# Performance work log

Hardware: AMD Instinct MI355X
Metric: run time of the kernel (lower is better)

## Reference

```python
import jax, jax.numpy as jnp
import numpy as np

B, R, E, H = 1024, 1024, 1024, 512
L_ATTR, L_OBJ, L_RELA = 16, 36, 64
EPS = 1e-8


def _lstm_cell(x, h, c, Wih, Whh, bih, bhh):
    # torch.nn.LSTMCell: gates ordered i, f, g, o
    g = x @ Wih.T + bih + h @ Whh.T + bhh
    i, f, gg, o = jnp.split(g, 4, axis=1)
    c2 = jax.nn.sigmoid(f) * c + jax.nn.sigmoid(i) * jnp.tanh(gg)
    h2 = jax.nn.sigmoid(o) * jnp.tanh(c2)
    return h2, c2


def _attend(h, feats, p_feats, mask, Wq, bq, wa, ba):
    att_h = h @ Wq.T + bq                         # [B,H]
    dot = jnp.tanh(p_feats + att_h[:, None, :])   # [B,L,H]
    scores = dot @ wa + ba                        # [B,L]
    w = jax.nn.softmax(scores, axis=1)
    w = w * mask
    w = w / (w.sum(1, keepdims=True) + EPS)
    return jnp.einsum('bl,bld->bd', w, feats)     # [B,R]


def setup_inputs() -> dict:
    key = jax.random.key(0)
    ks = iter(jax.random.split(key, 64))
    n = lambda shp, s=0.02: jax.random.normal(next(ks), shp, dtype=jnp.float32) * s
    inp = {
        'xt': n((B, E), 1.0), 'fc_feats': n((B, R), 1.0),
        'state_h': n((2, B, R), 1.0), 'state_c': n((2, B, R), 1.0),
        'attr_feats': n((B, L_ATTR, R), 1.0), 'obj_feats': n((B, L_OBJ, R), 1.0),
        'rela_feats': n((B, L_RELA, R), 1.0),
        'p_attr_feats': n((B, L_ATTR, H), 1.0), 'p_obj_feats': n((B, L_OBJ, H), 1.0),
        'p_rela_feats': n((B, L_RELA, H), 1.0),
        'attr_masks': jnp.ones((B, L_ATTR), jnp.float32),
        'att_masks': jnp.ones((B, L_OBJ), jnp.float32),
        'rela_masks': jnp.ones((B, L_RELA), jnp.float32),
        'att_Wih': n((4 * R, E + 2 * R)), 'att_Whh': n((4 * R, R)),
        'att_bih': n((4 * R,)), 'att_bhh': n((4 * R,)),
        'lang_Wih': n((4 * R, 4 * R)), 'lang_Whh': n((4 * R, R)),
        'lang_bih': n((4 * R,)), 'lang_bhh': n((4 * R,)),
    }
    for p in ('attr', 'obj', 'rela'):
        inp[p + '_Wq'] = n((H, R)); inp[p + '_bq'] = n((H,))
        inp[p + '_wa'] = n((H,));   inp[p + '_ba'] = n((1,))
    return inp


def reference(xt, fc_feats, state_h, state_c, attr_feats, obj_feats, rela_feats,
              p_attr_feats, p_obj_feats, p_rela_feats, attr_masks, att_masks,
              rela_masks, att_Wih, att_Whh, att_bih, att_bhh, lang_Wih, lang_Whh,
              lang_bih, lang_bhh, attr_Wq, attr_bq, attr_wa, attr_ba, obj_Wq,
              obj_bq, obj_wa, obj_ba, rela_Wq, rela_bq, rela_wa, rela_ba):
    prev_h = state_h[-1]
    att_in = jnp.concatenate([prev_h, fc_feats, xt], axis=1)
    h_att, c_att = _lstm_cell(att_in, state_h[0], state_c[0],
                              att_Wih, att_Whh, att_bih, att_bhh)
    a_attr = _attend(h_att, attr_feats, p_attr_feats, attr_masks,
                     attr_Wq, attr_bq, attr_wa, attr_ba)
    a_obj = _attend(h_att, obj_feats, p_obj_feats, att_masks,
                    obj_Wq, obj_bq, obj_wa, obj_ba)
    a_rela = _attend(h_att, rela_feats, p_rela_feats, rela_masks,
                     rela_Wq, rela_bq, rela_wa, rela_ba)
    lang_in = jnp.concatenate([h_att, a_attr, a_obj, a_rela], axis=1)
    h_lang, c_lang = _lstm_cell(lang_in, state_h[1], state_c[1],
                                lang_Wih, lang_Whh, lang_bih, lang_bhh)
    # dropout in eval mode -> identity
    output = h_lang
    return output, jnp.stack([h_att, h_lang]), jnp.stack([c_att, c_lang])
```

## Files before the change

kernel.cpp:

```cpp
#include <hip/hip_runtime.h>
#include <math.h>

typedef _Float16 half8  __attribute__((ext_vector_type(8)));
typedef _Float16 half4v __attribute__((ext_vector_type(4)));
typedef float    f32x4  __attribute__((ext_vector_type(4)));

__device__ __forceinline__ _Float16 f2h(float f) { return (_Float16)f; }

__device__ __forceinline__ float tanh_fast(float x) {
    float e = __expf(2.f * x);
    return 1.f - 2.f / (e + 1.f);
}

#define LDSB (128 * 40)

__device__ __forceinline__ void gemm_body(
    _Float16* __restrict__ sm,
    const float* A0, const float* A1, const float* A2p, const float* A3,
    const float* A4,
    const float* W0, const float* W1, const float* W2,
    int w0cols, int w0s, int w1s, int nsel,
    _Float16* __restrict__ Cpart, int ldc,
    int kb, int kLen, int ntile, int mtile, int zout)
{
    _Float16* smA = sm;
    _Float16* smW = sm + 2 * LDSB;
    const int tid  = threadIdx.x;
    const int lane = tid & 63;
    const int wid  = tid >> 6;
    const int wm   = wid >> 1, wn = wid & 1;
    const int m0   = mtile * 128;
    const int n0   = ntile * 128;
    const int nt   = kLen >> 5;
    const int srow = tid >> 3;
    const int scol = (tid & 7) << 2;
    const int fr   = lane & 15;
    const int kq   = lane >> 4;

    const float* wsel = nullptr;
    if (nsel) {
        int sel = n0 >> 9;
        const float* Wq = (sel == 0) ? W0 : (sel == 1) ? W1 : W2;
        wsel = Wq + (size_t)((n0 & 511) + srow) * 1024 + kb + scol;
    }

    f32x4 acc[4][4] = {};
    float4 va[4], vw[4];

    auto LOADA = [&](int lk) {
        int gk = kb + lk;
        int seg = gk >> 10;
        const float* ap = (seg == 0) ? A0 : (seg == 1) ? A1 : (seg == 2) ? A2p
                        : (seg == 3) ? A3 : A4;
        ap += (size_t)(m0 + srow) * 1024 + (gk & 1023) + scol;
        #pragma unroll
        for (int p = 0; p < 4; ++p)
            va[p] = *reinterpret_cast<const float4*>(ap + (size_t)p * 32 * 1024);
    };
    auto LOADW = [&](int lk) {
        const float* wp; int wstr;
        if (nsel) {
            wp = wsel + lk; wstr = 1024;
        } else {
            int gk = kb + lk;
            if (gk < w0cols) { wp = W0 + (size_t)(n0 + srow) * w0s + gk + scol;            wstr = w0s; }
            else             { wp = W1 + (size_t)(n0 + srow) * w1s + (gk - w0cols) + scol; wstr = w1s; }
        }
        #pragma unroll
        for (int p = 0; p < 4; ++p)
            vw[p] = *reinterpret_cast<const float4*>(wp + (size_t)p * 32 * wstr);
    };
    auto WRITEA = [&](int buf) {
        _Float16* d = smA + buf * LDSB;
        #pragma unroll
        for (int p = 0; p < 4; ++p) {
            half4v h = { f2h(va[p].x), f2h(va[p].y), f2h(va[p].z), f2h(va[p].w) };
            *reinterpret_cast<half4v*>(&d[(srow + p * 32) * 40 + scol]) = h;
        }
    };
    auto WRITEW = [&](int buf) {
        _Float16* d = smW + buf * LDSB;
        #pragma unroll
        for (int p = 0; p < 4; ++p) {
            half4v h = { f2h(vw[p].x), f2h(vw[p].y), f2h(vw[p].z), f2h(vw[p].w) };
            *reinterpret_cast<half4v*>(&d[(srow + p * 32) * 40 + scol]) = h;
        }
    };
    auto DOMFMA = [&](int buf) {
        half8 af[4], bf[4];
        _Float16* sA = smA + buf * LDSB;
        _Float16* sW = smW + buf * LDSB;
        #pragma unroll
        for (int i = 0; i < 4; ++i) {
            af[i] = *reinterpret_cast<const half8*>(&sA[(wm * 64 + i * 16 + fr) * 40 + kq * 8]);
            bf[i] = *reinterpret_cast<const half8*>(&sW[(wn * 64 + i * 16 + fr) * 40 + kq * 8]);
        }
        #pragma unroll
        for (int i = 0; i < 4; ++i)
            #pragma unroll
            for (int j = 0; j < 4; ++j)
                acc[i][j] = __builtin_amdgcn_mfma_f32_16x16x32_f16(af[i], bf[j], acc[i][j], 0, 0, 0);
    };

    LOADA(0); LOADW(0);
    WRITEA(0); WRITEW(0);
    __syncthreads();
    int cur = 0;
    for (int it = 0; it < nt - 1; ++it) {
        LOADA((it + 1) * 32);
        LOADW((it + 1) * 32);
        DOMFMA(cur);
        WRITEA(cur ^ 1);
        WRITEW(cur ^ 1);
        __syncthreads();
        cur ^= 1;
    }
    DOMFMA(cur);

    _Float16* cp = Cpart + (size_t)zout * 1024ull * (size_t)ldc;
    #pragma unroll
    for (int j = 0; j < 4; ++j) {
        int nc = n0 + wn * 64 + j * 16 + fr;
        #pragma unroll
        for (int i = 0; i < 4; ++i) {
            int rb = m0 + wm * 64 + i * 16 + kq * 4;
            #pragma unroll
            for (int r = 0; r < 4; ++r)
                cp[(size_t)(rb + r) * ldc + nc] = (_Float16)acc[i][j][r];
        }
    }
}

__global__ __launch_bounds__(256) void gemm_hf(
    const float* A0, const float* A1, const float* A2p, const float* A3,
    const float* A4,
    const float* W0, const float* W1, const float* W2,
    int w0cols, int w0s, int w1s, int nsel,
    _Float16* Cpart, int ldc, int kLen, int zbase)
{
    __shared__ _Float16 sm[4 * LDSB];
    gemm_body(sm, A0, A1, A2p, A3, A4, W0, W1, W2, w0cols, w0s, w1s, nsel,
              Cpart, ldc, blockIdx.z * kLen, kLen,
              blockIdx.x, blockIdx.y, zbase + blockIdx.z);
}

template<int L>
__device__ __forceinline__ void attend_mod(
    const float* __restrict__ feats,
    const float* __restrict__ pfeats,
    const float* __restrict__ mask,
    const _Float16* __restrict__ q0,
    const _Float16* __restrict__ q1,
    const float* __restrict__ bq, const float* __restrict__ wa,
    const float* __restrict__ ba,
    float* __restrict__ outa, int b,
    float* q, float* sc, float* wgt)
{
    const int tid = threadIdx.x;
    const int lane = tid & 63, wid = tid >> 6;
    for (int i = tid; i < 512; i += 256)
        q[i] = (float)q0[(size_t)b * 1536 + i] + (float)q1[(size_t)b * 1536 + i] + bq[i];
    __syncthreads();

    const float4* q4  = reinterpret_cast<const float4*>(q);
    const float4* wa4 = reinterpret_cast<const float4*>(wa);
    float4 qv0 = q4[lane],  qv1 = q4[lane + 64];
    float4 wv0 = wa4[lane], wv1 = wa4[lane + 64];
    const float ba0 = ba[0];
    const float4* pfb = reinterpret_cast<const float4*>(pfeats + (size_t)b * L * 512);

    auto score_row = [&](float4 a0, float4 a1) -> float {
        float s = tanh_fast(a0.x + qv0.x) * wv0.x
                + tanh_fast(a0.y + qv0.y) * wv0.y
                + tanh_fast(a0.z + qv0.z) * wv0.z
                + tanh_fast(a0.w + qv0.w) * wv0.w
                + tanh_fast(a1.x + qv1.x) * wv1.x
                + tanh_fast(a1.y + qv1.y) * wv1.y
                + tanh_fast(a1.z + qv1.z) * wv1.z
                + tanh_fast(a1.w + qv1.w) * wv1.w;
        #pragma unroll
        for (int off = 32; off >= 1; off >>= 1) s += __shfl_xor(s, off);
        return s;
    };

    constexpr int ROWS = L / 4;
    constexpr int QUADS = ROWS / 4;
    #pragma unroll
    for (int c = 0; c < QUADS; ++c) {
        float4 a0_[4], a1_[4];
        #pragma unroll
        for (int j = 0; j < 4; ++j) {
            const int l = wid + 4 * (c * 4 + j);
            a0_[j] = pfb[(size_t)l * 128 + lane];
            a1_[j] = pfb[(size_t)l * 128 + 64 + lane];
        }
        #pragma unroll
        for (int j = 0; j < 4; ++j) {
            const int l = wid + 4 * (c * 4 + j);
            float s = score_row(a0_[j], a1_[j]);
            if (lane == 0) sc[l] = s + ba0;
        }
    }
    #pragma unroll
    for (int r = QUADS * 4; r < ROWS; ++r) {
        const int l = wid + 4 * r;
        float4 a0 = pfb[(size_t)l * 128 + lane];
        float4 a1 = pfb[(size_t)l * 128 + 64 + lane];
        float s = score_row(a0, a1);
        if (lane == 0) sc[l] = s + ba0;
    }
    __syncthreads();

    if (tid < 64) {
        float v = (tid < L) ? sc[tid] : -1e30f;
        float m = v;
        #pragma unroll
        for (int off = 32; off >= 1; off >>= 1) m = fmaxf(m, __shfl_xor(m, off));
        float e = (tid < L) ? __expf(v - m) : 0.f;
        float sum = e;
        #pragma unroll
        for (int off = 32; off >= 1; off >>= 1) sum += __shfl_xor(sum, off);
        float w = e / sum;
        float wm = (tid < L) ? w * mask[(size_t)b * L + tid] : 0.f;
        float s2 = wm;
        #pragma unroll
        for (int off = 32; off >= 1; off >>= 1) s2 += __shfl_xor(s2, off);
        wgt[tid] = wm / (s2 + 1e-8f);
    }
    __syncthreads();

    const int d0 = tid * 4;
    const float* fp = feats + (size_t)b * L * 1024 + d0;
    f32x4 acc = {0.f, 0.f, 0.f, 0.f};
    constexpr int NFULL = L / 8;
    float4 vA[8], vB[8];

    #pragma unroll
    for (int j = 0; j < 8; ++j)
        vA[j] = *reinterpret_cast<const float4*>(fp + (size_t)j * 1024);
    #pragma unroll
    for (int g = 0; g < NFULL; ++g) {
        float4* cur = (g & 1) ? vB : vA;
        float4* nxt = (g & 1) ? vA : vB;
        if (g + 1 < NFULL) {
            #pragma unroll
            for (int j = 0; j < 8; ++j)
                nxt[j] = *reinterpret_cast<const float4*>(fp + (size_t)((g + 1) * 8 + j) * 1024);
        }
        #pragma unroll
        for (int j = 0; j < 8; ++j) {
            const float w = wgt[g * 8 + j];
            acc[0] += w * cur[j].x; acc[1] += w * cur[j].y;
            acc[2] += w * cur[j].z; acc[3] += w * cur[j].w;
        }
    }
    #pragma unroll
    for (int lg = NFULL * 8; lg < L; ++lg) {
        float4 v = *reinterpret_cast<const float4*>(fp + (size_t)lg * 1024);
        const float w = wgt[lg];
        acc[0] += w * v.x; acc[1] += w * v.y; acc[2] += w * v.z; acc[3] += w * v.w;
    }
    float4 o; o.x = acc[0]; o.y = acc[1]; o.z = acc[2]; o.w = acc[3];
    *reinterpret_cast<float4*>(outa + (size_t)b * 1024 + d0) = o;
}

__global__ __launch_bounds__(256) void attend3(
    const float* __restrict__ attr_feats, const float* __restrict__ obj_feats,
    const float* __restrict__ rela_feats,
    const float* __restrict__ p_attr, const float* __restrict__ p_obj,
    const float* __restrict__ p_rela,
    const float* __restrict__ attr_masks, const float* __restrict__ att_masks,
    const float* __restrict__ rela_masks,
    const _Float16* __restrict__ q16,
    const float* __restrict__ attr_bq, const float* __restrict__ obj_bq,
    const float* __restrict__ rela_bq,
    const float* __restrict__ attr_wa, const float* __restrict__ obj_wa,
    const float* __restrict__ rela_wa,
    const float* __restrict__ attr_ba, const float* __restrict__ obj_ba,
    const float* __restrict__ rela_ba,
    float* __restrict__ a32)
{
    __shared__ __align__(16) float q[512];
    __shared__ float sc[64];
    __shared__ float wgt[64];
    const int bid = blockIdx.x;
    const int mod = bid % 3;
    const int b   = bid / 3;
    const _Float16* q0 = q16 + mod * 512;
    const _Float16* q1 = q16 + 1536ull * 1024 + mod * 512;
    if (mod == 0)
        attend_mod<16>(attr_feats, p_attr, attr_masks, q0, q1,
                       attr_bq, attr_wa, attr_ba, a32, b, q, sc, wgt);
    else if (mod == 1)
        attend_mod<36>(obj_feats, p_obj, att_masks, q0, q1,
                       obj_bq, obj_wa, obj_ba, a32 + 1024ull * 1024, b, q, sc, wgt);
    else
        attend_mod<64>(rela_feats, p_rela, rela_masks, q0, q1,
                       rela_bq, rela_wa, rela_ba, a32 + 2ull * 1024 * 1024, b, q, sc, wgt);
}

__global__ __launch_bounds__(256) void lstm4(
    const _Float16* __restrict__ g, size_t zstride, int nz,
    const float* __restrict__ bih, const float* __restrict__ bhh,
    const float* __restrict__ c_prev,
    float* __restrict__ hA, float* __restrict__ hB,
    float* __restrict__ c_out)
{
    int idx = blockIdx.x * 256 + threadIdx.x;
    int b = idx >> 10, r = idx & 1023;
    size_t base = (size_t)b * 4096;
    float gi = bih[r]        + bhh[r];
    float gf = bih[1024 + r] + bhh[1024 + r];
    float gg = bih[2048 + r] + bhh[2048 + r];
    float go = bih[3072 + r] + bhh[3072 + r];
    for (int z = 0; z < nz; ++z) {
        const _Float16* gz = g + (size_t)z * zstride + base;
        gi += (float)gz[r];
        gf += (float)gz[1024 + r];
        gg += (float)gz[2048 + r];
        go += (float)gz[3072 + r];
    }
    float si = 1.f / (1.f + __expf(-gi));
    float sf = 1.f / (1.f + __expf(-gf));
    float so = 1.f / (1.f + __expf(-go));
    float c2 = sf * c_prev[idx] + si * tanh_fast(gg);
    float h2 = so * tanh_fast(c2);
    hA[idx] = h2;
    if (hB) hB[idx] = h2;
    c_out[idx] = c2;
}

extern "C" void kernel_launch(void* const* d_in, const int* in_sizes, int n_in,
                              void* d_out, int out_size, void* d_ws, size_t ws_size,
                              hipStream_t stream)
{
    const size_t BR = 1024ull * 1024ull;
    const float* xt         = (const float*)d_in[0];
    const float* fc         = (const float*)d_in[1];
    const float* state_h    = (const float*)d_in[2];
    const float* state_c    = (const float*)d_in[3];
    const float* attr_feats = (const float*)d_in[4];
    const float* obj_feats  = (const float*)d_in[5];
    const float* rela_feats = (const float*)d_in[6];
    const float* p_attr     = (const float*)d_in[7];
    const float* p_obj      = (const float*)d_in[8];
    const float* p_rela     = (const float*)d_in[9];
    const float* attr_masks = (const float*)d_in[10];
    const float* att_masks  = (const float*)d_in[11];
    const float* rela_masks = (const float*)d_in[12];
    const float* att_Wih    = (const float*)d_in[13];
    const float* att_Whh    = (const float*)d_in[14];
    const float* att_bih    = (const float*)d_in[15];
    const float* att_bhh    = (const float*)d_in[16];
    const float* lang_Wih   = (const float*)d_in[17];
    const float* lang_Whh   = (const float*)d_in[18];
    const float* lang_bih   = (const float*)d_in[19];
    const float* lang_bhh   = (const float*)d_in[20];
    const float* attr_Wq    = (const float*)d_in[21];
    const float* attr_bq    = (const float*)d_in[22];
    const float* attr_wa    = (const float*)d_in[23];
    const float* attr_ba    = (const float*)d_in[24];
    const float* obj_Wq     = (const float*)d_in[25];
    const float* obj_bq     = (const float*)d_in[26];
    const float* obj_wa     = (const float*)d_in[27];
    const float* obj_ba     = (const float*)d_in[28];
    const float* rela_Wq    = (const float*)d_in[29];
    const float* rela_bq    = (const float*)d_in[30];
    const float* rela_wa    = (const float*)d_in[31];
    const float* rela_ba    = (const float*)d_in[32];

    float* out = (float*)d_out;
    const float* h0 = state_h;
    const float* h1 = state_h + BR;
    float* h_att = out + BR;

    const bool big = ws_size >= 52428800ull;
    const int gslots = big ? 4 : 2;
    _Float16* g16 = (_Float16*)d_ws;
    _Float16* q16 = g16 + (size_t)gslots * 4ull * BR;
    float*    a32 = (float*)(q16 + 2ull * 1536 * 1024);
    float* a_attr = a32;
    float* a_obj  = a32 + BR;
    float* a_rela = a32 + 2 * BR;

    dim3 blk(256);
    const int zsplit = big ? 4 : 2;

    gemm_hf<<<dim3(32, 8, zsplit), blk, 0, stream>>>(
        h1, fc, xt, h0, h0, att_Wih, att_Whh, att_Whh,
        3072, 3072, 1024, 0, g16, 4096, 4096 / zsplit, 0);
    lstm4<<<dim3(4096), blk, 0, stream>>>(
        g16, 4ull * BR, gslots, att_bih, att_bhh, state_c,
        h_att, nullptr, out + 3 * BR);
    gemm_hf<<<dim3(12, 8, 2), blk, 0, stream>>>(
        h_att, h_att, h_att, h_att, h_att,
        attr_Wq, obj_Wq, rela_Wq, 0, 1024, 1024, 1,
        q16, 1536, 512, 0);
    attend3<<<dim3(3072), blk, 0, stream>>>(
        attr_feats, obj_feats, rela_feats, p_attr, p_obj, p_rela,
        attr_masks, att_masks, rela_masks, q16,
        attr_bq, obj_bq, rela_bq, attr_wa, obj_wa, rela_wa,
        attr_ba, obj_ba, rela_ba, a32);
    gemm_hf<<<dim3(32, 8, zsplit), blk, 0, stream>>>(
        h_att, a_attr, a_obj, a_rela, h1,
        lang_Wih, lang_Whh, lang_Whh, 4096, 4096, 1024, 0,
        g16, 4096, 5120 / zsplit, 0);
    lstm4<<<dim3(4096), blk, 0, stream>>>(
        g16, 4ull * BR, gslots, lang_bih, lang_bhh, state_c + BR,
        out, out + 2 * BR, out + 4 * BR);
}
```

Before: 428.1 us.

## Split fused attention kernel into scores, softmax, and weighted-sum kernels

```diff
diff --git a/kernel.cpp b/kernel.cpp
--- a/kernel.cpp
+++ b/kernel.cpp
@@ -144,97 +144,91 @@
               blockIdx.x, blockIdx.y, zbase + blockIdx.z);
 }
 
+
+__global__ __launch_bounds__(256) void att_scores(
+    const float* __restrict__ p_attr, const float* __restrict__ p_obj,
+    const float* __restrict__ p_rela,
+    const _Float16* __restrict__ q16,
+    const float* __restrict__ attr_bq, const float* __restrict__ obj_bq,
+    const float* __restrict__ rela_bq,
+    const float* __restrict__ attr_wa, const float* __restrict__ obj_wa,
+    const float* __restrict__ rela_wa,
+    const float* __restrict__ attr_ba, const float* __restrict__ obj_ba,
+    const float* __restrict__ rela_ba,
+    float* __restrict__ scg)
+{
+    const unsigned gw = blockIdx.x * 4u + (threadIdx.x >> 6);
+    const int lane = threadIdx.x & 63;
+    const unsigned b = gw / 116u;
+    const int r = (int)(gw - b * 116u);
+    const float* pf; const float* bq; const float* wa; const float* ba;
+    int l, moff, scoff, L;
+    if (r < 16)      { pf = p_attr; bq = attr_bq; wa = attr_wa; ba = attr_ba; l = r;      moff = 0;    scoff = 0;  L = 16; }
+    else if (r < 52) { pf = p_obj;  bq = obj_bq;  wa = obj_wa;  ba = obj_ba;  l = r - 16; moff = 512;  scoff = 16; L = 36; }
+    else             { pf = p_rela; bq = rela_bq; wa = rela_wa; ba = rela_ba; l = r - 52; moff = 1024; scoff = 52; L = 64; }
+
+    const float4* pf4 = reinterpret_cast<const float4*>(pf) + ((size_t)b * L + l) * 128 + lane * 2;
+    float4 a0 = pf4[0];
+    float4 a1 = pf4[1];
+    const _Float16* qb = q16 + (size_t)b * 1536 + moff + lane * 8;
+    half8 hq0 = *reinterpret_cast<const half8*>(qb);
+    half8 hq1 = *reinterpret_cast<const half8*>(qb + 1536ull * 1024);
+    const float4* bq4 = reinterpret_cast<const float4*>(bq) + lane * 2;
+    const float4* wa4 = reinterpret_cast<const float4*>(wa) + lane * 2;
+    float4 b0 = bq4[0], b1 = bq4[1];
+    float4 w0 = wa4[0], w1 = wa4[1];
+
+    float s = tanh_fast(a0.x + (float)hq0[0] + (float)hq1[0] + b0.x) * w0.x
+            + tanh_fast(a0.y + (float)hq0[1] + (float)hq1[1] + b0.y) * w0.y
+            + tanh_fast(a0.z + (float)hq0[2] + (float)hq1[2] + b0.z) * w0.z
+            + tanh_fast(a0.w + (float)hq0[3] + (float)hq1[3] + b0.w) * w0.w
+            + tanh_fast(a1.x + (float)hq0[4] + (float)hq1[4] + b1.x) * w1.x
+            + tanh_fast(a1.y + (float)hq0[5] + (float)hq1[5] + b1.y) * w1.y
+            + tanh_fast(a1.z + (float)hq0[6] + (float)hq1[6] + b1.z) * w1.z
+            + tanh_fast(a1.w + (float)hq0[7] + (float)hq1[7] + b1.w) * w1.w;
+    #pragma unroll
+    for (int off = 32; off >= 1; off >>= 1) s += __shfl_xor(s, off);
+    if (lane == 0) scg[(size_t)b * 128 + scoff + l] = s + ba[0];
+}
+
+__global__ __launch_bounds__(256) void att_softmax(
+    const float* __restrict__ scg,
+    const float* __restrict__ attr_masks, const float* __restrict__ att_masks,
+    const float* __restrict__ rela_masks,
+    float* __restrict__ wgtg)
+{
+    const int b = blockIdx.x;
+    const int wid = threadIdx.x >> 6, lane = threadIdx.x & 63;
+    if (wid >= 3) return;
+    const int L     = (wid == 0) ? 16 : (wid == 1) ? 36 : 64;
+    const int scoff = (wid == 0) ? 0  : (wid == 1) ? 16 : 52;
+    const float* mask = (wid == 0) ? attr_masks : (wid == 1) ? att_masks : rela_masks;
+    float v = (lane < L) ? scg[(size_t)b * 128 + scoff + lane] : -1e30f;
+    float m = v;
+    #pragma unroll
+    for (int off = 32; off >= 1; off >>= 1) m = fmaxf(m, __shfl_xor(m, off));
+    float e = (lane < L) ? __expf(v - m) : 0.f;
+    float sum = e;
+    #pragma unroll
+    for (int off = 32; off >= 1; off >>= 1) sum += __shfl_xor(sum, off);
+    float w = e / sum;
+    float wm = (lane < L) ? w * mask[(size_t)b * L + lane] : 0.f;
+    float s2 = wm;
+    #pragma unroll
+    for (int off = 32; off >= 1; off >>= 1) s2 += __shfl_xor(s2, off);
+    if (lane < L) wgtg[(size_t)b * 128 + scoff + lane] = wm / (s2 + 1e-8f);
+}
+
 template<int L>
-__device__ __forceinline__ void attend_mod(
-    const float* __restrict__ feats,
-    const float* __restrict__ pfeats,
-    const float* __restrict__ mask,
-    const _Float16* __restrict__ q0,
-    const _Float16* __restrict__ q1,
-    const float* __restrict__ bq, const float* __restrict__ wa,
-    const float* __restrict__ ba,
-    float* __restrict__ outa, int b,
-    float* q, float* sc, float* wgt)
-{
-    const int tid = threadIdx.x;
-    const int lane = tid & 63, wid = tid >> 6;
-    for (int i = tid; i < 512; i += 256)
-        q[i] = (float)q0[(size_t)b * 1536 + i] + (float)q1[(size_t)b * 1536 + i] + bq[i];
-    __syncthreads();
-
-    const float4* q4  = reinterpret_cast<const float4*>(q);
-    const float4* wa4 = reinterpret_cast<const float4*>(wa);
-    float4 qv0 = q4[lane],  qv1 = q4[lane + 64];
-    float4 wv0 = wa4[lane], wv1 = wa4[lane + 64];
-    const float ba0 = ba[0];
-    const float4* pfb = reinterpret_cast<const float4*>(pfeats + (size_t)b * L * 512);
-
-    auto score_row = [&](float4 a0, float4 a1) -> float {
-        float s = tanh_fast(a0.x + qv0.x) * wv0.x
-                + tanh_fast(a0.y + qv0.y) * wv0.y
-                + tanh_fast(a0.z + qv0.z) * wv0.z
-                + tanh_fast(a0.w + qv0.w) * wv0.w
-                + tanh_fast(a1.x + qv1.x) * wv1.x
-                + tanh_fast(a1.y + qv1.y) * wv1.y
-                + tanh_fast(a1.z + qv1.z) * wv1.z
-                + tanh_fast(a1.w + qv1.w) * wv1.w;
-        #pragma unroll
-        for (int off = 32; off >= 1; off >>= 1) s += __shfl_xor(s, off);
-        return s;
-    };
-
-    constexpr int ROWS = L / 4;
-    constexpr int QUADS = ROWS / 4;
-    #pragma unroll
-    for (int c = 0; c < QUADS; ++c) {
-        float4 a0_[4], a1_[4];
-        #pragma unroll
-        for (int j = 0; j < 4; ++j) {
-            const int l = wid + 4 * (c * 4 + j);
-            a0_[j] = pfb[(size_t)l * 128 + lane];
-            a1_[j] = pfb[(size_t)l * 128 + 64 + lane];
-        }
-        #pragma unroll
-        for (int j = 0; j < 4; ++j) {
-            const int l = wid + 4 * (c * 4 + j);
-            float s = score_row(a0_[j], a1_[j]);
-            if (lane == 0) sc[l] = s + ba0;
-        }
-    }
-    #pragma unroll
-    for (int r = QUADS * 4; r < ROWS; ++r) {
-        const int l = wid + 4 * r;
-        float4 a0 = pfb[(size_t)l * 128 + lane];
-        float4 a1 = pfb[(size_t)l * 128 + 64 + lane];
-        float s = score_row(a0, a1);
-        if (lane == 0) sc[l] = s + ba0;
-    }
-    __syncthreads();
-
-    if (tid < 64) {
-        float v = (tid < L) ? sc[tid] : -1e30f;
-        float m = v;
-        #pragma unroll
-        for (int off = 32; off >= 1; off >>= 1) m = fmaxf(m, __shfl_xor(m, off));
-        float e = (tid < L) ? __expf(v - m) : 0.f;
-        float sum = e;
-        #pragma unroll
-        for (int off = 32; off >= 1; off >>= 1) sum += __shfl_xor(sum, off);
-        float w = e / sum;
-        float wm = (tid < L) ? w * mask[(size_t)b * L + tid] : 0.f;
-        float s2 = wm;
-        #pragma unroll
-        for (int off = 32; off >= 1; off >>= 1) s2 += __shfl_xor(s2, off);
-        wgt[tid] = wm / (s2 + 1e-8f);
-    }
-    __syncthreads();
-
-    const int d0 = tid * 4;
+__device__ __forceinline__ void wsum_mod(
+    const float* __restrict__ feats, const float* __restrict__ wgt,
+    float* __restrict__ outa, int b)
+{
+    const int d0 = threadIdx.x * 4;
     const float* fp = feats + (size_t)b * L * 1024 + d0;
     f32x4 acc = {0.f, 0.f, 0.f, 0.f};
     constexpr int NFULL = L / 8;
     float4 vA[8], vB[8];
-
     #pragma unroll
     for (int j = 0; j < 8; ++j)
         vA[j] = *reinterpret_cast<const float4*>(fp + (size_t)j * 1024);
@@ -264,39 +258,21 @@
     *reinterpret_cast<float4*>(outa + (size_t)b * 1024 + d0) = o;
 }
 
-__global__ __launch_bounds__(256) void attend3(
+__global__ __launch_bounds__(256) void att_wsum(
     const float* __restrict__ attr_feats, const float* __restrict__ obj_feats,
     const float* __restrict__ rela_feats,
-    const float* __restrict__ p_attr, const float* __restrict__ p_obj,
-    const float* __restrict__ p_rela,
-    const float* __restrict__ attr_masks, const float* __restrict__ att_masks,
-    const float* __restrict__ rela_masks,
-    const _Float16* __restrict__ q16,
-    const float* __restrict__ attr_bq, const float* __restrict__ obj_bq,
-    const float* __restrict__ rela_bq,
-    const float* __restrict__ attr_wa, const float* __restrict__ obj_wa,
-    const float* __restrict__ rela_wa,
-    const float* __restrict__ attr_ba, const float* __restrict__ obj_ba,
-    const float* __restrict__ rela_ba,
+    const float* __restrict__ wgtg,
     float* __restrict__ a32)
 {
-    __shared__ __align__(16) float q[512];
-    __shared__ float sc[64];
-    __shared__ float wgt[64];
     const int bid = blockIdx.x;
     const int mod = bid % 3;
     const int b   = bid / 3;
-    const _Float16* q0 = q16 + mod * 512;
-    const _Float16* q1 = q16 + 1536ull * 1024 + mod * 512;
     if (mod == 0)
-        attend_mod<16>(attr_feats, p_attr, attr_masks, q0, q1,
-                       attr_bq, attr_wa, attr_ba, a32, b, q, sc, wgt);
+        wsum_mod<16>(attr_feats, wgtg + (size_t)b * 128 + 0,  a32, b);
     else if (mod == 1)
-        attend_mod<36>(obj_feats, p_obj, att_masks, q0, q1,
-                       obj_bq, obj_wa, obj_ba, a32 + 1024ull * 1024, b, q, sc, wgt);
+        wsum_mod<36>(obj_feats,  wgtg + (size_t)b * 128 + 16, a32 + 1024ull * 1024, b);
     else
-        attend_mod<64>(rela_feats, p_rela, rela_masks, q0, q1,
-                       rela_bq, rela_wa, rela_ba, a32 + 2ull * 1024 * 1024, b, q, sc, wgt);
+        wsum_mod<64>(rela_feats, wgtg + (size_t)b * 128 + 52, a32 + 2ull * 1024 * 1024, b);
 }
 
 __global__ __launch_bounds__(256) void lstm4(
@@ -373,6 +349,8 @@
     const float* h0 = state_h;
     const float* h1 = state_h + BR;
     float* h_att = out + BR;
+    float* scg  = out;
+    float* wgtg = out + 1024 * 128;
 
     const bool big = ws_size >= 52428800ull;
     const int gslots = big ? 4 : 2;
@@ -396,11 +374,14 @@
         h_att, h_att, h_att, h_att, h_att,
         attr_Wq, obj_Wq, rela_Wq, 0, 1024, 1024, 1,
         q16, 1536, 512, 0);
-    attend3<<<dim3(3072), blk, 0, stream>>>(
-        attr_feats, obj_feats, rela_feats, p_attr, p_obj, p_rela,
-        attr_masks, att_masks, rela_masks, q16,
+    att_scores<<<dim3(29696), blk, 0, stream>>>(
+        p_attr, p_obj, p_rela, q16,
         attr_bq, obj_bq, rela_bq, attr_wa, obj_wa, rela_wa,
-        attr_ba, obj_ba, rela_ba, a32);
+        attr_ba, obj_ba, rela_ba, scg);
+    att_softmax<<<dim3(1024), blk, 0, stream>>>(
+        scg, attr_masks, att_masks, rela_masks, wgtg);
+    att_wsum<<<dim3(3072), blk, 0, stream>>>(
+        attr_feats, obj_feats, rela_feats, wgtg, a32);
     gemm_hf<<<dim3(32, 8, zsplit), blk, 0, stream>>>(
         h_att, a_attr, a_obj, a_rela, h1,
         lang_Wih, lang_Whh, lang_Whh, 4096, 4096, 1024, 0,
```

Measured after the change: 433.2 us. Within noise of the previous version (+1.2%).
